# Kernel optimization log

Measured on AMD Instinct MI355X. Metric: run time of the kernel, lower is better.

## Reference

```python
import jax, jax.numpy as jnp
import numpy as np

RESOLUTION = 32
NORMALIZE = True
EPS = 0.0


def setup_inputs() -> dict:
    key = jax.random.key(0)
    k1, k2 = jax.random.split(key)
    B, C, N = 16, 64, 65536
    features = jax.random.normal(k1, (B, C, N), dtype=jnp.float32)
    coords = jax.random.normal(k2, (B, 3, N), dtype=jnp.float32)
    return {"features": features, "coords": coords}


def _voxelize(features, coords, R, normalize, eps):
    B, C, N = features.shape
    # center coords per cloud: [B,3,N]
    nc = coords - jnp.mean(coords, axis=2, keepdims=True)
    if normalize:
        # max L2 norm over points -> [B,1,1]
        m = jnp.max(jnp.linalg.norm(nc, axis=1, keepdims=True), axis=2, keepdims=True)
        nc = nc / (m * 2.0 + eps) + 0.5
    else:
        nc = (nc + 1.0) / 2.0
    nc = jnp.clip(nc * R, 0.0, R - 1)                     # [B,3,N] in [0,R-1]
    vox = jnp.round(nc).astype(jnp.int32)                 # integer voxel coords
    # flatten voxel index: x*R^2 + y*R + z, then offset by batch
    idx = (vox[:, 0] * R + vox[:, 1]) * R + vox[:, 2]     # [B,N]
    flat_idx = (idx + jnp.arange(B, dtype=jnp.int32)[:, None] * (R ** 3)).reshape(-1)
    # scatter-add features and counts per voxel
    feats_t = features.transpose(0, 2, 1).reshape(B * N, C)
    sums = jax.ops.segment_sum(feats_t, flat_idx, num_segments=B * R ** 3)  # [B*R^3, C]
    cnt = jax.ops.segment_sum(jnp.ones((B * N,), features.dtype), flat_idx,
                              num_segments=B * R ** 3)                      # [B*R^3]
    avg = sums / jnp.maximum(cnt, 1.0)[:, None]
    grid = avg.reshape(B, R, R, R, C).transpose(0, 4, 1, 2, 3)              # [B,C,R,R,R]
    return grid, nc


def reference(features, coords):
    return _voxelize(features, coords, RESOLUTION, NORMALIZE, EPS)
```

## Files before the change

### kernel.cpp

```cpp
#include <hip/hip_runtime.h>

#define NB   16
#define NC   64
#define NPTS 65536
#define RES  32
#define R3   32768
#define PPB  2048

typedef float fx4 __attribute__((ext_vector_type(4)));
typedef int   ix4 __attribute__((ext_vector_type(4)));

__global__ void mean_partial(const float* __restrict__ coords, float* __restrict__ meanacc) {
    int bid = blockIdx.x;
    int b = bid >> 5, chunk = bid & 31;
    const float* cb = coords + (size_t)b * 3 * NPTS + chunk * PPB;
    float s0 = 0.f, s1 = 0.f, s2 = 0.f;
    for (int i = threadIdx.x; i < PPB; i += 256) {
        s0 += cb[i];
        s1 += cb[NPTS + i];
        s2 += cb[2 * NPTS + i];
    }
    for (int off = 32; off > 0; off >>= 1) {
        s0 += __shfl_down(s0, off);
        s1 += __shfl_down(s1, off);
        s2 += __shfl_down(s2, off);
    }
    if ((threadIdx.x & 63) == 0) {
        atomicAdd(&meanacc[b * 3 + 0], s0);
        atomicAdd(&meanacc[b * 3 + 1], s1);
        atomicAdd(&meanacc[b * 3 + 2], s2);
    }
}

__global__ void maxnorm_partial(const float* __restrict__ coords,
                                const float* __restrict__ meanacc,
                                int* __restrict__ maxn) {
    int bid = blockIdx.x;
    int b = bid >> 5, chunk = bid & 31;
    const float* cb = coords + (size_t)b * 3 * NPTS + chunk * PPB;
    float m0 = meanacc[b * 3 + 0] * (1.0f / NPTS);
    float m1 = meanacc[b * 3 + 1] * (1.0f / NPTS);
    float m2 = meanacc[b * 3 + 2] * (1.0f / NPTS);
    float mx = 0.f;
    for (int i = threadIdx.x; i < PPB; i += 256) {
        float x = cb[i] - m0;
        float y = cb[NPTS + i] - m1;
        float z = cb[2 * NPTS + i] - m2;
        mx = fmaxf(mx, sqrtf(x * x + y * y + z * z));
    }
    for (int off = 32; off > 0; off >>= 1)
        mx = fmaxf(mx, __shfl_down(mx, off));
    if ((threadIdx.x & 63) == 0)
        atomicMax(&maxn[b], __float_as_int(mx));
}

__global__ void voxelize(const float* __restrict__ coords,
                         const float* __restrict__ meanacc,
                         const int* __restrict__ maxn,
                         float* __restrict__ ncout,
                         unsigned short* __restrict__ voxid,
                         unsigned int* __restrict__ cnt) {
    int t = blockIdx.x * 256 + threadIdx.x;
    int b = t >> 16, n = t & (NPTS - 1);
    const float* cb = coords + (size_t)b * 3 * NPTS;
    float m2 = __int_as_float(maxn[b]) * 2.0f;
    float c0 = meanacc[b * 3 + 0] * (1.0f / NPTS);
    float c1 = meanacc[b * 3 + 1] * (1.0f / NPTS);
    float c2 = meanacc[b * 3 + 2] * (1.0f / NPTS);
    float ncx = (cb[n]            - c0) / m2 + 0.5f;
    float ncy = (cb[NPTS + n]     - c1) / m2 + 0.5f;
    float ncz = (cb[2 * NPTS + n] - c2) / m2 + 0.5f;
    float sx = fminf(fmaxf(ncx * (float)RES, 0.f), (float)(RES - 1));
    float sy = fminf(fmaxf(ncy * (float)RES, 0.f), (float)(RES - 1));
    float sz = fminf(fmaxf(ncz * (float)RES, 0.f), (float)(RES - 1));
    float* nb = ncout + (size_t)b * 3 * NPTS;
    __builtin_nontemporal_store(sx, &nb[n]);
    __builtin_nontemporal_store(sy, &nb[NPTS + n]);
    __builtin_nontemporal_store(sz, &nb[2 * NPTS + n]);
    int v = (((int)rintf(sx)) << 10) + (((int)rintf(sy)) << 5) + (int)rintf(sz);
    voxid[t] = (unsigned short)v;
    atomicAdd(&cnt[((size_t)b << 15) + v], 1u);
}

__global__ __launch_bounds__(1024) void lds_grid(const float* __restrict__ features,
                                                 const unsigned short* __restrict__ voxid,
                                                 const unsigned int* __restrict__ cnt,
                                                 float* __restrict__ grid) {
    extern __shared__ int acc[];
    int b = blockIdx.x >> 6, c = blockIdx.x & 63;
    ix4* a4 = (ix4*)acc;
    for (int i = threadIdx.x; i < (R3 >> 2); i += 1024)
        a4[i] = (ix4){0, 0, 0, 0};
    __syncthreads();
    const fx4*     f4 = (const fx4*)(features + ((size_t)((b << 6) + c) << 16));
    const ushort4* v4 = (const ushort4*)(voxid + ((size_t)b << 16));
    fx4     f0 = __builtin_nontemporal_load(&f4[threadIdx.x]);
    fx4     f1 = __builtin_nontemporal_load(&f4[threadIdx.x + 1024]);
    ushort4 u0 = v4[threadIdx.x];
    ushort4 u1 = v4[threadIdx.x + 1024];
#pragma unroll
    for (int j = 0; j < 16; ++j) {
        fx4     fn = f1;
        ushort4 vn = u1;
        if (j < 14) {
            fn = __builtin_nontemporal_load(&f4[threadIdx.x + ((j + 2) << 10)]);
            vn = v4[threadIdx.x + ((j + 2) << 10)];
        }
        atomicAdd(&acc[u0.x], (int)rintf(f0.x * 65536.0f));
        atomicAdd(&acc[u0.y], (int)rintf(f0.y * 65536.0f));
        atomicAdd(&acc[u0.z], (int)rintf(f0.z * 65536.0f));
        atomicAdd(&acc[u0.w], (int)rintf(f0.w * 65536.0f));
        f0 = f1; u0 = u1;
        f1 = fn; u1 = vn;
    }
    __syncthreads();
    const uint4* cb4 = (const uint4*)(cnt + ((size_t)b << 15));
    fx4* g4 = (fx4*)(grid + ((size_t)((b << 6) + c) << 15));
    for (int i = threadIdx.x; i < (R3 >> 2); i += 1024) {
        ix4   a = a4[i];
        uint4 k = cb4[i];
        fx4 o;
        o.x = (float)a.x * (1.0f / 65536.0f) / fmaxf((float)k.x, 1.0f);
        o.y = (float)a.y * (1.0f / 65536.0f) / fmaxf((float)k.y, 1.0f);
        o.z = (float)a.z * (1.0f / 65536.0f) / fmaxf((float)k.z, 1.0f);
        o.w = (float)a.w * (1.0f / 65536.0f) / fmaxf((float)k.w, 1.0f);
        __builtin_nontemporal_store(o, &g4[i]);
    }
}

extern "C" void kernel_launch(void* const* d_in, const int* in_sizes, int n_in,
                              void* d_out, int out_size, void* d_ws, size_t ws_size,
                              hipStream_t stream) {
    const float* features = (const float*)d_in[0];
    const float* coords   = (const float*)d_in[1];

    float* grid  = (float*)d_out;
    float* ncout = grid + (size_t)NB * NC * R3;

    char* base = (char*)d_ws;
    float* meanacc = (float*)base;
    int*   maxn    = (int*)(base + 192);
    unsigned int*   cnt   = (unsigned int*)(base + 256);
    unsigned short* voxid = (unsigned short*)(cnt + (size_t)NB * R3);

    hipMemsetAsync(d_ws, 0, 256 + (size_t)NB * R3 * sizeof(unsigned int), stream);

    mean_partial   <<<NB * 32, 256, 0, stream>>>(coords, meanacc);
    maxnorm_partial<<<NB * 32, 256, 0, stream>>>(coords, meanacc, maxn);
    voxelize       <<<NB * NPTS / 256, 256, 0, stream>>>(coords, meanacc, maxn, ncout, voxid, cnt);
    lds_grid       <<<NB * NC, 1024, R3 * sizeof(int), stream>>>(features, voxid, cnt, grid);
}
```

Measured before the change: 518.3 us.

## Process four channels per block, caching voxel ids in registers, XCD-aware mapping

The LDS scatter kernel now runs 256 blocks, each handling four consecutive channels of one batch instead of one. The voxel ids for the batch are loaded once into registers and reused across the four channel passes. The feature prefetch pipeline also runs across pass boundaries. Block-to-batch mapping is arranged so blocks sharing the same XCD work on the same batches, which should improve L2 reuse of voxid and cnt. The trade-off is fewer blocks (256, about one per CU), extra syncs per pass, and more register pressure from holding 16 ushort4 values, so occupancy and latency hiding may suffer.

```diff
diff --git a/kernel.cpp b/kernel.cpp
--- a/kernel.cpp
+++ b/kernel.cpp
@@ -87,44 +87,59 @@
                                                  const unsigned int* __restrict__ cnt,
                                                  float* __restrict__ grid) {
     extern __shared__ int acc[];
-    int b = blockIdx.x >> 6, c = blockIdx.x & 63;
+    int blk = blockIdx.x;
+    int xcd = blk & 7, slot = blk >> 3;
+    int b   = (xcd << 1) + (slot >> 4);
+    int cb_ = (slot & 15) << 2;
+    int tid = threadIdx.x;
     ix4* a4 = (ix4*)acc;
-    for (int i = threadIdx.x; i < (R3 >> 2); i += 1024)
-        a4[i] = (ix4){0, 0, 0, 0};
-    __syncthreads();
-    const fx4*     f4 = (const fx4*)(features + ((size_t)((b << 6) + c) << 16));
+
     const ushort4* v4 = (const ushort4*)(voxid + ((size_t)b << 16));
-    fx4     f0 = __builtin_nontemporal_load(&f4[threadIdx.x]);
-    fx4     f1 = __builtin_nontemporal_load(&f4[threadIdx.x + 1024]);
-    ushort4 u0 = v4[threadIdx.x];
-    ushort4 u1 = v4[threadIdx.x + 1024];
+    ushort4 us[16];
 #pragma unroll
-    for (int j = 0; j < 16; ++j) {
-        fx4     fn = f1;
-        ushort4 vn = u1;
-        if (j < 14) {
-            fn = __builtin_nontemporal_load(&f4[threadIdx.x + ((j + 2) << 10)]);
-            vn = v4[threadIdx.x + ((j + 2) << 10)];
+    for (int j = 0; j < 16; ++j)
+        us[j] = v4[tid + (j << 10)];
+
+    const fx4* fbase = (const fx4*)(features + ((size_t)((b << 6) + cb_) << 16));
+    const uint4* cb4 = (const uint4*)(cnt + ((size_t)b << 15));
+
+    fx4 f0 = __builtin_nontemporal_load(&fbase[tid]);
+    fx4 f1 = __builtin_nontemporal_load(&fbase[tid + 1024]);
+
+    for (int p = 0; p < 4; ++p) {
+        for (int i = tid; i < (R3 >> 2); i += 1024)
+            a4[i] = (ix4){0, 0, 0, 0};
+        __syncthreads();
+        const fx4* f4  = fbase + ((size_t)p << 14);
+        const fx4* f4n = fbase + ((size_t)(p + 1) << 14);
+#pragma unroll
+        for (int j = 0; j < 16; ++j) {
+            fx4 fn = f1;
+            if (j < 14)
+                fn = __builtin_nontemporal_load(&f4[tid + ((j + 2) << 10)]);
+            else if (p < 3)
+                fn = __builtin_nontemporal_load(&f4n[tid + ((j - 14) << 10)]);
+            ushort4 u = us[j];
+            atomicAdd(&acc[u.x], (int)rintf(f0.x * 65536.0f));
+            atomicAdd(&acc[u.y], (int)rintf(f0.y * 65536.0f));
+            atomicAdd(&acc[u.z], (int)rintf(f0.z * 65536.0f));
+            atomicAdd(&acc[u.w], (int)rintf(f0.w * 65536.0f));
+            f0 = f1;
+            f1 = fn;
         }
-        atomicAdd(&acc[u0.x], (int)rintf(f0.x * 65536.0f));
-        atomicAdd(&acc[u0.y], (int)rintf(f0.y * 65536.0f));
-        atomicAdd(&acc[u0.z], (int)rintf(f0.z * 65536.0f));
-        atomicAdd(&acc[u0.w], (int)rintf(f0.w * 65536.0f));
-        f0 = f1; u0 = u1;
-        f1 = fn; u1 = vn;
-    }
-    __syncthreads();
-    const uint4* cb4 = (const uint4*)(cnt + ((size_t)b << 15));
-    fx4* g4 = (fx4*)(grid + ((size_t)((b << 6) + c) << 15));
-    for (int i = threadIdx.x; i < (R3 >> 2); i += 1024) {
-        ix4   a = a4[i];
-        uint4 k = cb4[i];
-        fx4 o;
-        o.x = (float)a.x * (1.0f / 65536.0f) / fmaxf((float)k.x, 1.0f);
-        o.y = (float)a.y * (1.0f / 65536.0f) / fmaxf((float)k.y, 1.0f);
-        o.z = (float)a.z * (1.0f / 65536.0f) / fmaxf((float)k.z, 1.0f);
-        o.w = (float)a.w * (1.0f / 65536.0f) / fmaxf((float)k.w, 1.0f);
-        __builtin_nontemporal_store(o, &g4[i]);
+        __syncthreads();
+        fx4* g4 = (fx4*)(grid + ((size_t)((b << 6) + cb_ + p) << 15));
+        for (int i = tid; i < (R3 >> 2); i += 1024) {
+            ix4   a = a4[i];
+            uint4 k = cb4[i];
+            fx4 o;
+            o.x = (float)a.x * (1.0f / 65536.0f) / fmaxf((float)k.x, 1.0f);
+            o.y = (float)a.y * (1.0f / 65536.0f) / fmaxf((float)k.y, 1.0f);
+            o.z = (float)a.z * (1.0f / 65536.0f) / fmaxf((float)k.z, 1.0f);
+            o.w = (float)a.w * (1.0f / 65536.0f) / fmaxf((float)k.w, 1.0f);
+            __builtin_nontemporal_store(o, &g4[i]);
+        }
+        __syncthreads();
     }
 }
 
@@ -148,5 +163,5 @@
     mean_partial   <<<NB * 32, 256, 0, stream>>>(coords, meanacc);
     maxnorm_partial<<<NB * 32, 256, 0, stream>>>(coords, meanacc, maxn);
     voxelize       <<<NB * NPTS / 256, 256, 0, stream>>>(coords, meanacc, maxn, ncout, voxid, cnt);
-    lds_grid       <<<NB * NC, 1024, R3 * sizeof(int), stream>>>(features, voxid, cnt, grid);
+    lds_grid       <<<256, 1024, R3 * sizeof(int), stream>>>(features, voxid, cnt, grid);
 }
```

Result: no change. 516.5 us (-0.3%).
